# Kernel optimization log

Hardware: AMD Instinct MI355X
Metric: run time of the kernel (lower is better)

Reference implementation:

```python
import math
import jax, jax.numpy as jnp
import numpy as np

T, B, C, H = 1024, 4, 1024, 16
D = C // H  # d_k = 64


def setup_inputs() -> dict:
    key = jax.random.key(0)
    ks = jax.random.split(key, 16)
    s = 0.02
    return {
        "query": jax.random.normal(ks[0], (T, B, C), jnp.float32),
        "key": jax.random.normal(ks[1], (T, B, C), jnp.float32),
        "value": jax.random.normal(ks[2], (T, B, C), jnp.float32),
        "pos_emb": jax.random.normal(ks[3], (2 * T - 1, 1, C), jnp.float32),
        "Wq": jax.random.normal(ks[4], (C, C), jnp.float32) * s,
        "bq": jnp.zeros((C,), jnp.float32),
        "Wk": jax.random.normal(ks[5], (C, C), jnp.float32) * s,
        "bk": jnp.zeros((C,), jnp.float32),
        "Wv": jax.random.normal(ks[6], (C, C), jnp.float32) * s,
        "bv": jnp.zeros((C,), jnp.float32),
        "Wp": jax.random.normal(ks[7], (C, C), jnp.float32) * s,
        "Wo": jax.random.normal(ks[8], (C, C), jnp.float32) * s,
        "bo": jnp.zeros((C,), jnp.float32),
        "pos_bias_u": jax.random.normal(ks[9], (H, D), jnp.float32) * s,
        "pos_bias_v": jax.random.normal(ks[10], (H, D), jnp.float32) * s,
    }


def rel_shift(x):
    # x: [B, H, T, P] with P = 2T-1 -> [B, H, T, T]
    b, h, t, p = x.shape
    x = jnp.pad(x, ((0, 0), (0, 0), (0, 0), (1, 0)))  # [B,H,T,P+1]
    x = x.reshape(b, h, p + 1, t)[:, :, 1:, :].reshape(b, h, t, p)
    return x[..., : p // 2 + 1]


def reference(query, key, value, pos_emb, Wq, bq, Wk, bk, Wv, bv, Wp, Wo, bo,
              pos_bias_u, pos_bias_v):
    # T x B x C -> B x T x C
    q_in = query.transpose(1, 0, 2)
    k_in = key.transpose(1, 0, 2)
    v_in = value.transpose(1, 0, 2)
    p_in = pos_emb.transpose(1, 0, 2)  # [1, 2T-1, C]

    q = (q_in @ Wq.T + bq).reshape(B, T, H, D)            # [B,T,H,D]
    k = (k_in @ Wk.T + bk).reshape(B, T, H, D)
    v = (v_in @ Wv.T + bv).reshape(B, T, H, D)
    p = (p_in @ Wp.T).reshape(2 * T - 1, H, D)            # [2T-1,H,D]

    # content (ac) and position (bd) scores
    matrix_ac = jnp.einsum('bthd,bshd->bhts', q + pos_bias_u, k)   # [B,H,T,T]
    matrix_bd = jnp.einsum('bthd,phd->bhtp', q + pos_bias_v, p)    # [B,H,T,2T-1]
    matrix_bd = rel_shift(matrix_bd)                               # [B,H,T,T]

    scores = (matrix_ac + matrix_bd) / math.sqrt(D)
    scores = jnp.clip(scores, -1e8, 1e8)
    attn = jax.nn.softmax(scores.astype(jnp.float32), axis=-1).astype(scores.dtype)

    x = jnp.einsum('bhts,bshd->bthd', attn, v).reshape(B, T, C)
    out = x @ Wo.T + bo
    return out.transpose(1, 0, 2)  # T x B x C
```

## Files before the change

kernel.cpp:

```cpp
#include <hip/hip_runtime.h>
#include <hip/hip_bf16.h>
#include <math.h>

#define T_SEQ 1024
#define NB 4
#define NH 16
#define DD 64
#define CC 1024

typedef __attribute__((ext_vector_type(8))) short short8;
typedef __attribute__((ext_vector_type(4))) float floatx4;
typedef __attribute__((ext_vector_type(4))) unsigned short ushort4v;

#define MFMA(a, b, c) __builtin_amdgcn_mfma_f32_16x16x32_bf16((a), (b), (c), 0, 0, 0)

__device__ inline float bf2f(unsigned short u) {
  union { unsigned int i; float f; } c; c.i = ((unsigned int)u) << 16; return c.f;
}
__device__ inline unsigned short f2bf(float x) {
  union { float f; unsigned int i; } c; c.f = x;
  unsigned int u = c.i;
  u += 0x7fff + ((u >> 16) & 1);
  return (unsigned short)(u >> 16);
}

__device__ __forceinline__ void gload_lds16(const void* g, void* l) {
  __builtin_amdgcn_global_load_lds(
      (const __attribute__((address_space(1))) unsigned int*)g,
      (__attribute__((address_space(3))) unsigned int*)l, 16, 0, 0);
}

__global__ __launch_bounds__(256) void convert_kernel(
    const float* __restrict__ q, const float* __restrict__ k,
    const float* __restrict__ v, const float* __restrict__ pe_in,
    const float* __restrict__ wq, const float* __restrict__ wk,
    const float* __restrict__ wv, const float* __restrict__ wp,
    const float* __restrict__ wo,
    unsigned short* __restrict__ qo, unsigned short* __restrict__ ko,
    unsigned short* __restrict__ vo, unsigned short* __restrict__ po,
    unsigned short* __restrict__ wqo, unsigned short* __restrict__ wko,
    unsigned short* __restrict__ wvo, unsigned short* __restrict__ wpo,
    unsigned short* __restrict__ woo)
{
  const int i = blockIdx.x * 256 + threadIdx.x;
  const float* src; unsigned short* dst; int off;
  if      (i < 524288)  { src = q;     dst = qo;  off = i; }
  else if (i < 1048576) { src = k;     dst = ko;  off = i - 524288; }
  else if (i < 1572864) { src = v;     dst = vo;  off = i - 1048576; }
  else if (i < 1834880) { src = pe_in; dst = po;  off = i - 1572864; }
  else if (i < 1965952) { src = wq;    dst = wqo; off = i - 1834880; }
  else if (i < 2097024) { src = wk;    dst = wko; off = i - 1965952; }
  else if (i < 2228096) { src = wv;    dst = wvo; off = i - 2097024; }
  else if (i < 2359168) { src = wp;    dst = wpo; off = i - 2228096; }
  else if (i < 2490240) { src = wo;    dst = woo; off = i - 2359168; }
  else {
    const int j = i - 2490240;
    *(short8*)&po[2047 * 1024 + j * 8] = (short8){0, 0, 0, 0, 0, 0, 0, 0};
    return;
  }
  const float4 a0 = *(const float4*)(src + (size_t)off * 8);
  const float4 a1 = *(const float4*)(src + (size_t)off * 8 + 4);
  short8 val = (short8){(short)f2bf(a0.x), (short)f2bf(a0.y), (short)f2bf(a0.z), (short)f2bf(a0.w),
                        (short)f2bf(a1.x), (short)f2bf(a1.y), (short)f2bf(a1.z), (short)f2bf(a1.w)};
  *(short8*)&dst[(size_t)off * 8] = val;
}

template <int OUT_BF16>
__device__ __forceinline__ void gemm_core_db(
    const unsigned short* __restrict__ A, const unsigned short* __restrict__ Wt,
    const float* __restrict__ bias, void* __restrict__ Cv,
    unsigned short* As0, unsigned short* Bs0,
    unsigned short* As1, unsigned short* Bs1,
    int N, int K, int bm, int bn)
{
  const int tid = threadIdx.x;
  const int lane = tid & 63;
  const int w = tid >> 6;
  const int l15 = lane & 15, quad = lane >> 4;
  const int rw = (w >> 1) * 64, cw = (w & 1) * 64;

  floatx4 acc[4][4];
#pragma unroll
  for (int i = 0; i < 4; ++i)
#pragma unroll
    for (int j = 0; j < 4; ++j) acc[i][j] = (floatx4){0.f, 0.f, 0.f, 0.f};

  const int lrow = lane >> 2, lcol = (lane & 3) * 8;
  const unsigned short* Ag = A + (size_t)(bm + w * 32 + lrow) * K + lcol;
  const unsigned short* Wg = Wt + (size_t)(bn + w * 32 + lrow) * K + lcol;

#define G_STAGE(AS, BS, KOFF)                                   \
  do {                                                          \
    gload_lds16(Ag + (KOFF), (AS) + w * 1024);                  \
    gload_lds16(Ag + 16 * K + (KOFF), (AS) + w * 1024 + 512);   \
    gload_lds16(Wg + (KOFF), (BS) + w * 1024);                  \
    gload_lds16(Wg + 16 * K + (KOFF), (BS) + w * 1024 + 512);   \
  } while (0)

#define G_COMPUTE(AS, BS)                                               \
  do {                                                                  \
    short8 af[4], bfr[4];                                               \
    _Pragma("unroll")                                                   \
    for (int i = 0; i < 4; ++i)                                         \
      af[i] = *(short8*)&(AS)[(rw + i * 16 + l15) * 32 + quad * 8];     \
    _Pragma("unroll")                                                   \
    for (int j = 0; j < 4; ++j)                                         \
      bfr[j] = *(short8*)&(BS)[(cw + j * 16 + l15) * 32 + quad * 8];    \
    _Pragma("unroll")                                                   \
    for (int i = 0; i < 4; ++i)                                         \
      _Pragma("unroll")                                                 \
      for (int j = 0; j < 4; ++j)                                       \
        acc[i][j] = MFMA(af[i], bfr[j], acc[i][j]);                     \
  } while (0)

  G_STAGE(As0, Bs0, 0);
  __syncthreads();

  for (int k0 = 0; k0 < K; k0 += 64) {
    if (k0 + 32 < K) G_STAGE(As1, Bs1, k0 + 32);
    G_COMPUTE(As0, Bs0);
    __syncthreads();
    if (k0 + 64 < K) G_STAGE(As0, Bs0, k0 + 64);
    G_COMPUTE(As1, Bs1);
    __syncthreads();
  }
#undef G_STAGE
#undef G_COMPUTE

#pragma unroll
  for (int j = 0; j < 4; ++j) {
    const int col = bn + cw + j * 16 + l15;
    const float bj = bias ? bias[col] : 0.f;
#pragma unroll
    for (int i = 0; i < 4; ++i) {
      const int row0 = bm + rw + i * 16 + quad * 4;
#pragma unroll
      for (int reg = 0; reg < 4; ++reg) {
        const float v = acc[i][j][reg] + bj;
        if (OUT_BF16)
          ((unsigned short*)Cv)[(size_t)(row0 + reg) * N + col] = f2bf(v);
        else
          ((float*)Cv)[(size_t)(row0 + reg) * N + col] = v;
      }
    }
  }
}

struct GemmJob { const unsigned short* A; const unsigned short* Wt;
                 const float* bias; unsigned short* C; int mtiles; };
struct GemmJobs { GemmJob j[4]; };

__global__ __launch_bounds__(256) void gemm_qkvp(GemmJobs jobs) {
  __shared__ __align__(16) unsigned short As0[128 * 32];
  __shared__ __align__(16) unsigned short Bs0[128 * 32];
  __shared__ __align__(16) unsigned short As1[128 * 32];
  __shared__ __align__(16) unsigned short Bs1[128 * 32];
  GemmJob jb = jobs.j[blockIdx.z];
  if ((int)blockIdx.y >= jb.mtiles) return;
  gemm_core_db<1>(jb.A, jb.Wt, jb.bias, jb.C, As0, Bs0, As1, Bs1,
                  1024, 1024, blockIdx.y * 128, blockIdx.x * 128);
}

template <int OUT_BF16>
__global__ __launch_bounds__(256) void gemm_one(
    const unsigned short* __restrict__ A, const unsigned short* __restrict__ Wt,
    const float* __restrict__ bias, void* __restrict__ Cv) {
  __shared__ __align__(16) unsigned short As0[128 * 32];
  __shared__ __align__(16) unsigned short Bs0[128 * 32];
  __shared__ __align__(16) unsigned short As1[128 * 32];
  __shared__ __align__(16) unsigned short Bs1[128 * 32];
  gemm_core_db<OUT_BF16>(A, Wt, bias, Cv, As0, Bs0, As1, Bs1,
                         1024, 1024, blockIdx.y * 128, blockIdx.x * 128);
}

__global__ __launch_bounds__(256) void transpose_precompute(
    const unsigned short* __restrict__ vb, unsigned short* __restrict__ vT,
    const unsigned short* __restrict__ kb, const unsigned short* __restrict__ pb,
    const float* __restrict__ pbu, const float* __restrict__ pbv,
    float* __restrict__ uk, float* __restrict__ vp)
{
  __shared__ __align__(16) unsigned short Lt[64 * 136];
  const int bid = blockIdx.x;
  const int tid = threadIdx.x;
  if (bid < 512) {
    const int t0 = (bid & 7) * 128;
    const int h = (bid >> 3) & 15, b = bid >> 7;
#pragma unroll
    for (int cc = 0; cc < 4; ++cc) {
      const int idx = tid + cc * 256;
      const int r = idx >> 3, pc = idx & 7;
      short8 val = *(const short8*)(vb + ((size_t)((t0 + r) * 4 + b)) * 1024 + h * 64 + pc * 8);
#pragma unroll
      for (int e = 0; e < 8; ++e)
        Lt[(pc * 8 + e) * 136 + r] = (unsigned short)val[e];
    }
    __syncthreads();
#pragma unroll
    for (int cc = 0; cc < 4; ++cc) {
      const int idx = tid + cc * 256;
      const int d = idx >> 4, tc = idx & 15;
      short8 v2 = *(short8*)&Lt[d * 136 + tc * 8];
      *(short8*)(vT + ((size_t)((b * 16 + h) * 64 + d)) * 1024 + t0 + tc * 8) = v2;
    }
  } else {
    const int i = (bid - 512) * 256 + tid;
    if (i < 65536) {
      const int b = i >> 14, h = (i >> 10) & 15, s = i & 1023;
      const unsigned short* kr = kb + ((size_t)(s * 4 + b)) * 1024 + h * 64;
      const float* ur = pbu + h * 64;
      float sum = 0.f;
#pragma unroll
      for (int c = 0; c < 8; ++c) {
        short8 kv = *(const short8*)(kr + c * 8);
#pragma unroll
        for (int e = 0; e < 8; ++e) sum += bf2f((unsigned short)kv[e]) * ur[c * 8 + e];
      }
      uk[i] = sum;
    } else if (i < 98304) {
      const int j = i - 65536;
      const int idx = j >> 4, h = j & 15;
      const unsigned short* pr = pb + (size_t)idx * 1024 + h * 64;
      const float* vr = pbv + h * 64;
      float sum = 0.f;
#pragma unroll
      for (int c = 0; c < 8; ++c) {
        short8 pv = *(const short8*)(pr + c * 8);
#pragma unroll
        for (int e = 0; e < 8; ++e) sum += bf2f((unsigned short)pv[e]) * vr[c * 8 + e];
      }
      vp[(idx << 4) + h] = sum;
    }
  }
}

#define BDW 148

__global__ __launch_bounds__(256) void attn_kernel(
    const unsigned short* __restrict__ qb, const unsigned short* __restrict__ kb,
    const unsigned short* __restrict__ pb, const unsigned short* __restrict__ vT,
    const float* __restrict__ uk, const float* __restrict__ vp,
    unsigned short* __restrict__ xb)
{
  __shared__ __align__(16) float SMEM_ALL[10240];
  float* BDf  = SMEM_ALL;
  unsigned short* Pb = (unsigned short*)SMEM_ALL;
  float* uk_s  = SMEM_ALL + 9472;
  float* vp_w  = SMEM_ALL + 9600;
  float* pmax0 = SMEM_ALL + 9792;
  float* pmax1 = SMEM_ALL + 9856;
  float* psum0 = SMEM_ALL + 9920;
  float* psum1 = SMEM_ALL + 9984;
  float* m_rowA = SMEM_ALL + 10048;
  float* m_rowB = SMEM_ALL + 10112;
  float* l_row  = SMEM_ALL + 10176;

  const int tid = threadIdx.x;
  const int lane = tid & 63;
  const int w = tid >> 6;
  const int l15 = lane & 15, quad = lane >> 4;
  const int th = w & 1, sh = w >> 1;

  const int flat = blockIdx.x + (blockIdx.y << 4) + (blockIdx.z << 8);
  const int x8 = flat & 7, s8 = flat >> 3;
  const int hb = x8 * 8 + (s8 >> 4);
  const int t0 = (s8 & 15) * 64;
  const int b = hb >> 4, h = hb & 15;

  short8 qf[2][2];
#pragma unroll
  for (int tt = 0; tt < 2; ++tt)
#pragma unroll
    for (int kk = 0; kk < 2; ++kk) {
      const int t = t0 + th * 32 + tt * 16 + l15;
      qf[tt][kk] = *(const short8*)(qb + ((size_t)(t * 4 + b)) * 1024 + h * 64 + kk * 32 + quad * 8);
    }

  floatx4 of[2][2];
#pragma unroll
  for (int i = 0; i < 2; ++i)
#pragma unroll
    for (int j = 0; j < 2; ++j) of[i][j] = (floatx4){0.f, 0.f, 0.f, 0.f};

  if (tid < 64) { m_rowA[tid] = -3.0e38f; l_row[tid] = 0.f; }
  __syncthreads();

  const unsigned short* kbase = kb + ((size_t)((sh * 64 + l15) * 4 + b)) * 1024 + h * 64;
  const unsigned short* pbase0 = pb + ((size_t)(sh * 96 + l15)) * 1024 + h * 64;

  short8 kf[4][2], pf[6][2];
  {
    const int w0 = 0 - t0 + 960;
#pragma unroll
    for (int st4 = 0; st4 < 4; ++st4) {
      const unsigned short* kr = kbase + (size_t)(st4 * 16) * 4096;
      kf[st4][0] = *(const short8*)(kr + quad * 8);
      kf[st4][1] = *(const short8*)(kr + 32 + quad * 8);
    }
#pragma unroll
    for (int jt = 0; jt < 6; ++jt) {
      const int sA = sh * 96 + jt * 16 + th * 32;
      if (sA <= 16 || sA > 190) continue;
      const unsigned short* pr = pbase0 + (size_t)(w0 + jt * 16) * 1024;
      pf[jt][0] = *(const short8*)(pr + quad * 8);
      pf[jt][1] = *(const short8*)(pr + 32 + quad * 8);
    }
  }

  for (int s0 = 0; s0 < 1024; s0 += 128) {
    const int w0 = s0 - t0 + 960;
    const int par = (s0 >> 7) & 1;
    float* m_prev = par ? m_rowB : m_rowA;
    float* m_next = par ? m_rowA : m_rowB;

    if (tid < 128) uk_s[tid] = uk[((b * 16 + h) << 10) + s0 + tid];
    if (tid < 192) vp_w[tid] = vp[(((size_t)(w0 + tid)) << 4) + h];

#pragma unroll
    for (int jt = 0; jt < 6; ++jt) {
      const int jjbase = sh * 96 + jt * 16;
#pragma unroll
      for (int tt = 0; tt < 2; ++tt) {
        const int tbase = th * 32 + tt * 16;
        const int ssum = jjbase + tbase;
        if (ssum <= 32 || ssum > 190) continue;
        floatx4 z = (floatx4){0.f, 0.f, 0.f, 0.f};
        z = MFMA(pf[jt][0], qf[tt][0], z);
        z = MFMA(pf[jt][1], qf[tt][1], z);
        const int tloc = tbase + l15;
        *(float4*)&BDf[tloc * BDW + (ssum - 48) + quad * 4] =
            make_float4(z[0], z[1], z[2], z[3]);
      }
    }

    floatx4 st[4][2];
#pragma unroll
    for (int stile = 0; stile < 4; ++stile) {
#pragma unroll
      for (int tt = 0; tt < 2; ++tt) {
        floatx4 z = (floatx4){0.f, 0.f, 0.f, 0.f};
        z = MFMA(kf[stile][0], qf[tt][0], z);
        z = MFMA(kf[stile][1], qf[tt][1], z);
        st[stile][tt] = z;
      }
    }

    {
      const int s0n = (s0 + 128 < 1024) ? (s0 + 128) : 0;
      const int w0n = s0n - t0 + 960;
#pragma unroll
      for (int st4 = 0; st4 < 4; ++st4) {
        const unsigned short* kr = kbase + (size_t)(s0n + st4 * 16) * 4096;
        kf[st4][0] = *(const short8*)(kr + quad * 8);
        kf[st4][1] = *(const short8*)(kr + 32 + quad * 8);
      }
#pragma unroll
      for (int jt = 0; jt < 6; ++jt) {
        const int sA = sh * 96 + jt * 16 + th * 32;
        if (sA <= 16 || sA > 190) continue;
        const unsigned short* pr = pbase0 + (size_t)(w0n + jt * 16) * 1024;
        pf[jt][0] = *(const short8*)(pr + quad * 8);
        pf[jt][1] = *(const short8*)(pr + 32 + quad * 8);
      }
    }
    __syncthreads();

    float lmax[2] = {-3.0e38f, -3.0e38f};
#pragma unroll
    for (int stile = 0; stile < 4; ++stile)
#pragma unroll
      for (int tt = 0; tt < 2; ++tt) {
        const int tloc = th * 32 + tt * 16 + l15;
#pragma unroll
        for (int reg = 0; reg < 4; ++reg) {
          const int sloc = sh * 64 + stile * 16 + quad * 4 + reg;
          const int jj = sloc - tloc + 63;
          float v = 0.125f * (st[stile][tt][reg] + BDf[tloc * BDW + sloc - l15 + 15] +
                              uk_s[sloc] + vp_w[jj]);
          st[stile][tt][reg] = v;
          lmax[tt] = fmaxf(lmax[tt], v);
        }
      }
#pragma unroll
    for (int tt = 0; tt < 2; ++tt) {
      lmax[tt] = fmaxf(lmax[tt], __shfl_xor(lmax[tt], 16));
      lmax[tt] = fmaxf(lmax[tt], __shfl_xor(lmax[tt], 32));
    }
    if (quad == 0) {
      float* pm = sh ? pmax1 : pmax0;
      pm[th * 32 + l15] = lmax[0];
      pm[th * 32 + 16 + l15] = lmax[1];
    }
    __syncthreads();

    float mn_keep = 0.f;
    if (tid < 64) {
      const float mo = m_prev[tid];
      mn_keep = fmaxf(mo, fmaxf(pmax0[tid], pmax1[tid]));
      m_next[tid] = mn_keep;
    }
    float mt[2];
#pragma unroll
    for (int tt = 0; tt < 2; ++tt) {
      const int r = th * 32 + tt * 16 + l15;
      mt[tt] = fmaxf(m_prev[r], fmaxf(pmax0[r], pmax1[r]));
    }

    float lsum[2] = {0.f, 0.f};
#pragma unroll
    for (int stile = 0; stile < 4; ++stile)
#pragma unroll
      for (int tt = 0; tt < 2; ++tt) {
        float p0 = __expf(st[stile][tt][0] - mt[tt]);
        float p1 = __expf(st[stile][tt][1] - mt[tt]);
        float p2 = __expf(st[stile][tt][2] - mt[tt]);
        float p3 = __expf(st[stile][tt][3] - mt[tt]);
        lsum[tt] += p0 + p1 + p2 + p3;
        const int tloc = th * 32 + tt * 16 + l15;
        const int sb = sh * 64 + stile * 16 + quad * 4;
        ushort4v pk = (ushort4v){f2bf(p0), f2bf(p1), f2bf(p2), f2bf(p3)};
        *(ushort4v*)&Pb[tloc * 136 + sb] = pk;
      }
#pragma unroll
    for (int tt = 0; tt < 2; ++tt) {
      lsum[tt] += __shfl_xor(lsum[tt], 16);
      lsum[tt] += __shfl_xor(lsum[tt], 32);
    }
    if (quad == 0) {
      float* ps = sh ? psum1 : psum0;
      ps[th * 32 + l15] = lsum[0];
      ps[th * 32 + 16 + l15] = lsum[1];
    }
#pragma unroll
    for (int tt = 0; tt < 2; ++tt) {
      const int base = th * 32 + tt * 16 + quad * 4;
      const float4 mo4 = *(const float4*)&m_prev[base];
      const float4 p04 = *(const float4*)&pmax0[base];
      const float4 p14 = *(const float4*)&pmax1[base];
#pragma unroll
      for (int reg = 0; reg < 4; ++reg) {
        const float mo = ((const float*)&mo4)[reg];
        const float mn = fmaxf(mo, fmaxf(((const float*)&p04)[reg],
                                         ((const float*)&p14)[reg]));
        const float ar = __expf(mo - mn);
        of[tt][0][reg] *= ar;
        of[tt][1][reg] *= ar;
      }
    }
    __syncthreads();

    if (tid < 64) {
      const float alpha = __expf(m_prev[tid] - mn_keep);
      l_row[tid] = l_row[tid] * alpha + psum0[tid] + psum1[tid];
    }
#pragma unroll
    for (int kk2 = 0; kk2 < 4; ++kk2) {
      short8 pa[2], vf[2];
#pragma unroll
      for (int tt = 0; tt < 2; ++tt)
        pa[tt] = *(short8*)&Pb[(th * 32 + tt * 16 + l15) * 136 + kk2 * 32 + quad * 8];
#pragma unroll
      for (int dt = 0; dt < 2; ++dt)
        vf[dt] = *(const short8*)(vT + ((size_t)((b * 16 + h) * 64 + sh * 32 + dt * 16 + l15)) * 1024 +
                                  s0 + kk2 * 32 + quad * 8);
#pragma unroll
      for (int tt = 0; tt < 2; ++tt)
#pragma unroll
        for (int dt = 0; dt < 2; ++dt)
          of[tt][dt] = MFMA(pa[tt], vf[dt], of[tt][dt]);
    }
    __syncthreads();
  }

#pragma unroll
  for (int tt = 0; tt < 2; ++tt)
#pragma unroll
    for (int reg = 0; reg < 4; ++reg) {
      const int t = th * 32 + tt * 16 + quad * 4 + reg;
      const float il = 1.f / l_row[t];
#pragma unroll
      for (int dt = 0; dt < 2; ++dt) {
        const int d = sh * 32 + dt * 16 + l15;
        xb[((size_t)((t0 + t) * 4 + b)) * 1024 + h * 64 + d] = f2bf(of[tt][dt][reg] * il);
      }
    }
}

extern "C" void kernel_launch(void* const* d_in, const int* in_sizes, int n_in,
                              void* d_out, int out_size, void* d_ws, size_t ws_size,
                              hipStream_t stream) {
  const float* query   = (const float*)d_in[0];
  const float* key_    = (const float*)d_in[1];
  const float* value   = (const float*)d_in[2];
  const float* pos_emb = (const float*)d_in[3];
  const float* Wq  = (const float*)d_in[4];
  const float* bq  = (const float*)d_in[5];
  const float* Wk  = (const float*)d_in[6];
  const float* bk  = (const float*)d_in[7];
  const float* Wv  = (const float*)d_in[8];
  const float* bv  = (const float*)d_in[9];
  const float* Wp  = (const float*)d_in[10];
  const float* Wo  = (const float*)d_in[11];
  const float* bo  = (const float*)d_in[12];
  const float* pbu = (const float*)d_in[13];
  const float* pbv = (const float*)d_in[14];
  float* out = (float*)d_out;

  unsigned short* U = (unsigned short*)d_ws;
  unsigned short* qin = U;
  unsigned short* kin = U + 4194304;
  unsigned short* vin = U + 8388608;
  unsigned short* pe  = U + 12582912;
  unsigned short* wq  = U + 14680064;
  unsigned short* wk  = U + 15728640;
  unsigned short* wv  = U + 16777216;
  unsigned short* wp  = U + 17825792;
  unsigned short* wo  = U + 18874368;
  unsigned short* qb  = U + 19922944;
  unsigned short* kb  = U + 24117248;
  unsigned short* pb  = U + 28311552;
  unsigned short* vpo = U + 30408704;
  unsigned short* vTb = pe;
  unsigned short* xb  = qin;
  float* fbase = (float*)(U + 34603008);
  float* uk = fbase;
  float* vp = fbase + 65536;

  const dim3 blk(256);

  convert_kernel<<<dim3(9728), blk, 0, stream>>>(
      query, key_, value, pos_emb, Wq, Wk, Wv, Wp, Wo,
      qin, kin, vin, pe, wq, wk, wv, wp, wo);

  GemmJobs jobs;
  jobs.j[0] = GemmJob{qin, wq, bq, qb, 32};
  jobs.j[1] = GemmJob{kin, wk, bk, kb, 32};
  jobs.j[2] = GemmJob{vin, wv, bv, vpo, 32};
  jobs.j[3] = GemmJob{pe,  wp, nullptr, pb, 16};
  gemm_qkvp<<<dim3(8, 32, 4), blk, 0, stream>>>(jobs);

  transpose_precompute<<<dim3(896), blk, 0, stream>>>(
      vpo, vTb, kb, pb, pbu, pbv, uk, vp);

  attn_kernel<<<dim3(16, 16, 4), blk, 0, stream>>>(qb, kb, pb, vTb, uk, vp, xb);

  gemm_one<0><<<dim3(8, 32), blk, 0, stream>>>(xb, wo, bo, out);
}
```

Before: 331.2 us.

## Deepen GEMM K-loop pipeline to four LDS stages with vmcnt-based waits

Replaces the double-buffered GEMM core with a four-stage ring of LDS buffers. Loads are issued two stages ahead, and each stage waits with a partial s_waitcnt vmcnt plus a raw barrier instead of a full __syncthreads. The aim is to hide global-to-LDS load latency in the projection GEMMs. LDS use doubles to 64KB per block, which can lower occupancy, and correctness depends on the hand-counted vmcnt values.

```diff
diff --git a/kernel.cpp b/kernel.cpp
--- a/kernel.cpp
+++ b/kernel.cpp
@@ -66,12 +66,10 @@
 }
 
 template <int OUT_BF16>
-__device__ __forceinline__ void gemm_core_db(
+__device__ __forceinline__ void gemm_core_p4(
     const unsigned short* __restrict__ A, const unsigned short* __restrict__ Wt,
     const float* __restrict__ bias, void* __restrict__ Cv,
-    unsigned short* As0, unsigned short* Bs0,
-    unsigned short* As1, unsigned short* Bs1,
-    int N, int K, int bm, int bn)
+    unsigned short* SM, int N, int K, int bm, int bn)
 {
   const int tid = threadIdx.x;
   const int lane = tid & 63;
@@ -89,23 +87,33 @@
   const unsigned short* Ag = A + (size_t)(bm + w * 32 + lrow) * K + lcol;
   const unsigned short* Wg = Wt + (size_t)(bn + w * 32 + lrow) * K + lcol;
 
-#define G_STAGE(AS, BS, KOFF)                                   \
-  do {                                                          \
-    gload_lds16(Ag + (KOFF), (AS) + w * 1024);                  \
-    gload_lds16(Ag + 16 * K + (KOFF), (AS) + w * 1024 + 512);   \
-    gload_lds16(Wg + (KOFF), (BS) + w * 1024);                  \
-    gload_lds16(Wg + 16 * K + (KOFF), (BS) + w * 1024 + 512);   \
+#define ASX(i) (SM + (i) * 4096)
+#define BSX(i) (SM + 16384 + (i) * 4096)
+
+#define G_STAGE(i, KOFF)                                            \
+  do {                                                              \
+    gload_lds16(Ag + (KOFF), ASX(i) + w * 1024);                    \
+    gload_lds16(Ag + 16 * K + (KOFF), ASX(i) + w * 1024 + 512);     \
+    gload_lds16(Wg + (KOFF), BSX(i) + w * 1024);                    \
+    gload_lds16(Wg + 16 * K + (KOFF), BSX(i) + w * 1024 + 512);     \
   } while (0)
 
-#define G_COMPUTE(AS, BS)                                               \
+#define G_WAITBAR(NN)                                               \
+  do {                                                              \
+    asm volatile("s_waitcnt vmcnt(" #NN ")" ::: "memory");          \
+    __builtin_amdgcn_s_barrier();                                   \
+    __builtin_amdgcn_sched_barrier(0);                              \
+  } while (0)
+
+#define G_COMPUTE(bi)                                                   \
   do {                                                                  \
     short8 af[4], bfr[4];                                               \
     _Pragma("unroll")                                                   \
     for (int i = 0; i < 4; ++i)                                         \
-      af[i] = *(short8*)&(AS)[(rw + i * 16 + l15) * 32 + quad * 8];     \
+      af[i] = *(short8*)&(ASX(bi))[(rw + i * 16 + l15) * 32 + quad * 8];\
     _Pragma("unroll")                                                   \
     for (int j = 0; j < 4; ++j)                                         \
-      bfr[j] = *(short8*)&(BS)[(cw + j * 16 + l15) * 32 + quad * 8];    \
+      bfr[j] = *(short8*)&(BSX(bi))[(cw + j * 16 + l15) * 32 + quad * 8];\
     _Pragma("unroll")                                                   \
     for (int i = 0; i < 4; ++i)                                         \
       _Pragma("unroll")                                                 \
@@ -113,19 +121,25 @@
         acc[i][j] = MFMA(af[i], bfr[j], acc[i][j]);                     \
   } while (0)
 
-  G_STAGE(As0, Bs0, 0);
-  __syncthreads();
-
-  for (int k0 = 0; k0 < K; k0 += 64) {
-    if (k0 + 32 < K) G_STAGE(As1, Bs1, k0 + 32);
-    G_COMPUTE(As0, Bs0);
-    __syncthreads();
-    if (k0 + 64 < K) G_STAGE(As0, Bs0, k0 + 64);
-    G_COMPUTE(As1, Bs1);
-    __syncthreads();
+  G_STAGE(0, 0);
+  G_STAGE(1, 32);
+
+  for (int k0 = 0; k0 < K - 128; k0 += 128) {
+    G_STAGE(2, k0 + 64);  G_WAITBAR(8); G_COMPUTE(0);
+    G_STAGE(3, k0 + 96);  G_WAITBAR(8); G_COMPUTE(1);
+    G_STAGE(0, k0 + 128); G_WAITBAR(8); G_COMPUTE(2);
+    G_STAGE(1, k0 + 160); G_WAITBAR(8); G_COMPUTE(3);
   }
+  G_STAGE(2, K - 64);  G_WAITBAR(8); G_COMPUTE(0);
+  G_STAGE(3, K - 32);  G_WAITBAR(8); G_COMPUTE(1);
+  G_WAITBAR(4); G_COMPUTE(2);
+  G_WAITBAR(0); G_COMPUTE(3);
+
 #undef G_STAGE
+#undef G_WAITBAR
 #undef G_COMPUTE
+#undef ASX
+#undef BSX
 
 #pragma unroll
   for (int j = 0; j < 4; ++j) {
@@ -151,26 +165,20 @@
 struct GemmJobs { GemmJob j[4]; };
 
 __global__ __launch_bounds__(256) void gemm_qkvp(GemmJobs jobs) {
-  __shared__ __align__(16) unsigned short As0[128 * 32];
-  __shared__ __align__(16) unsigned short Bs0[128 * 32];
-  __shared__ __align__(16) unsigned short As1[128 * 32];
-  __shared__ __align__(16) unsigned short Bs1[128 * 32];
+  __shared__ __align__(16) unsigned short SM[8 * 4096];
   GemmJob jb = jobs.j[blockIdx.z];
   if ((int)blockIdx.y >= jb.mtiles) return;
-  gemm_core_db<1>(jb.A, jb.Wt, jb.bias, jb.C, As0, Bs0, As1, Bs1,
-                  1024, 1024, blockIdx.y * 128, blockIdx.x * 128);
+  gemm_core_p4<1>(jb.A, jb.Wt, jb.bias, jb.C, SM, 1024, 1024,
+                  blockIdx.y * 128, blockIdx.x * 128);
 }
 
 template <int OUT_BF16>
 __global__ __launch_bounds__(256) void gemm_one(
     const unsigned short* __restrict__ A, const unsigned short* __restrict__ Wt,
     const float* __restrict__ bias, void* __restrict__ Cv) {
-  __shared__ __align__(16) unsigned short As0[128 * 32];
-  __shared__ __align__(16) unsigned short Bs0[128 * 32];
-  __shared__ __align__(16) unsigned short As1[128 * 32];
-  __shared__ __align__(16) unsigned short Bs1[128 * 32];
-  gemm_core_db<OUT_BF16>(A, Wt, bias, Cv, As0, Bs0, As1, Bs1,
-                         1024, 1024, blockIdx.y * 128, blockIdx.x * 128);
+  __shared__ __align__(16) unsigned short SM[8 * 4096];
+  gemm_core_p4<OUT_BF16>(A, Wt, bias, Cv, SM, 1024, 1024,
+                         blockIdx.y * 128, blockIdx.x * 128);
 }
 
 __global__ __launch_bounds__(256) void transpose_precompute(
```

Result: faster. 317.9 us (-4.0%).
